# Performance work log

Hardware: AMD Instinct MI355X
Metric: run time of the kernel (lower is better)

Reference implementation:

```python
import jax, jax.numpy as jnp
import numpy as np

INPUT_SIZE = 256
HIDDEN = 64
VOCAB = 8000
B, T = 64, 256


def _lstm_layer(x_seq, W_ih, W_hh, b_ih, b_hh):
    # x_seq: [B, T, D_in]; PyTorch gate order: i, f, g, o
    Bsz = x_seq.shape[0]
    H = W_hh.shape[1]
    # Precompute input projections for all timesteps (one big GEMM)
    x_proj = jnp.einsum('btd,gd->btg', x_seq, W_ih) + b_ih + b_hh  # [B,T,4H]

    def step(carry, xt):
        h, c = carry
        gates = xt + h @ W_hh.T  # [B,4H]
        i, f, g, o = jnp.split(gates, 4, axis=-1)
        i = jax.nn.sigmoid(i)
        f = jax.nn.sigmoid(f)
        g = jnp.tanh(g)
        o = jax.nn.sigmoid(o)
        c = f * c + i * g
        h = o * jnp.tanh(c)
        return (h, c), h

    zeros = jnp.zeros((Bsz, H), x_seq.dtype)
    _, hs = jax.lax.scan(step, (zeros, zeros), jnp.swapaxes(x_proj, 0, 1))
    return jnp.swapaxes(hs, 0, 1)  # [B,T,H]


def setup_inputs() -> dict:
    key = jax.random.key(0)
    ks = jax.random.split(key, 12)
    s0 = 1.0 / np.sqrt(HIDDEN)
    x = jax.random.normal(ks[0], (B, T, INPUT_SIZE), dtype=jnp.float32)
    W_ih0 = jax.random.uniform(ks[1], (4 * HIDDEN, INPUT_SIZE), jnp.float32, -s0, s0)
    W_hh0 = jax.random.uniform(ks[2], (4 * HIDDEN, HIDDEN), jnp.float32, -s0, s0)
    b_ih0 = jax.random.uniform(ks[3], (4 * HIDDEN,), jnp.float32, -s0, s0)
    b_hh0 = jax.random.uniform(ks[4], (4 * HIDDEN,), jnp.float32, -s0, s0)
    W_ih1 = jax.random.uniform(ks[5], (4 * HIDDEN, HIDDEN), jnp.float32, -s0, s0)
    W_hh1 = jax.random.uniform(ks[6], (4 * HIDDEN, HIDDEN), jnp.float32, -s0, s0)
    b_ih1 = jax.random.uniform(ks[7], (4 * HIDDEN,), jnp.float32, -s0, s0)
    b_hh1 = jax.random.uniform(ks[8], (4 * HIDDEN,), jnp.float32, -s0, s0)
    Wl = jax.random.uniform(ks[9], (VOCAB, HIDDEN), jnp.float32, -s0, s0)
    bl = jax.random.uniform(ks[10], (VOCAB,), jnp.float32, -s0, s0)
    return {"x": x, "W_ih0": W_ih0, "W_hh0": W_hh0, "b_ih0": b_ih0, "b_hh0": b_hh0,
            "W_ih1": W_ih1, "W_hh1": W_hh1, "b_ih1": b_ih1, "b_hh1": b_hh1,
            "Wl": Wl, "bl": bl}


def reference(x, W_ih0, W_hh0, b_ih0, b_hh0, W_ih1, W_hh1, b_ih1, b_hh1, Wl, bl):
    h1 = _lstm_layer(x, W_ih0, W_hh0, b_ih0, b_hh0)   # [B,T,H]
    h2 = _lstm_layer(h1, W_ih1, W_hh1, b_ih1, b_hh1)  # [B,T,H]
    return jnp.einsum('bth,vh->btv', h2, Wl) + bl      # [B,T,VOCAB]
```

## Files before the change

kernel.cpp:

```cpp
#include <hip/hip_runtime.h>
#include <math.h>

#define HID 64
#define G4 256
#define TSTEPS 256
#define BATCH 64
#define MTOT 16384
#define NVOCAB 8000

__device__ __forceinline__ float tanh_s(float x){
    float ax = fabsf(x);
    float e = __expf(-2.0f*ax);
    float t = (1.0f - e)/(1.0f + e);
    return x >= 0.f ? t : -t;
}

__global__ void bsum_k(const float* __restrict__ a, const float* __restrict__ b, float* __restrict__ o, int n){
    int i = blockIdx.x*256 + threadIdx.x;
    if (i < n) o[i] = a[i] + b[i];
}

template<int KTOT>
__global__ __launch_bounds__(256, 2) void gemm_bias_nt(
    const float* __restrict__ A, const float* __restrict__ B,
    const float* __restrict__ bias, float* __restrict__ C,
    int M, int N)
{
    __shared__ float As[64][132];
    __shared__ float Bs[64][132];
    const int tid = threadIdx.x;
    const int tx = tid & 15;
    const int ty = tid >> 4;
    const int m0 = blockIdx.y * 128;
    const int n0 = blockIdx.x * 128;

    float4 acc0[8], acc1[8];
    #pragma unroll
    for (int i = 0; i < 8; i++){
        acc0[i] = make_float4(0.f,0.f,0.f,0.f);
        acc1[i] = make_float4(0.f,0.f,0.f,0.f);
    }

    const int rl = tid & 15;
    const int k4 = (tid >> 4) * 4;

    for (int k0 = 0; k0 < KTOT; k0 += 64){
        #pragma unroll
        for (int it = 0; it < 8; it++){
            int r = it*16 + rl;
            float4 va = *(const float4*)(A + (size_t)(m0+r)*KTOT + k0 + k4);
            As[k4+0][r] = va.x; As[k4+1][r] = va.y;
            As[k4+2][r] = va.z; As[k4+3][r] = va.w;
            float4 vb = make_float4(0.f,0.f,0.f,0.f);
            if (n0 + r < N)
                vb = *(const float4*)(B + (size_t)(n0+r)*KTOT + k0 + k4);
            Bs[k4+0][r] = vb.x; Bs[k4+1][r] = vb.y;
            Bs[k4+2][r] = vb.z; Bs[k4+3][r] = vb.w;
        }
        __syncthreads();

        #pragma unroll 8
        for (int k = 0; k < 64; k++){
            float4 a0 = *(const float4*)&As[k][ty*8];
            float4 a1 = *(const float4*)&As[k][ty*8 + 4];
            float4 b0 = *(const float4*)&Bs[k][tx*4];
            float4 b1 = *(const float4*)&Bs[k][64 + tx*4];
            float av[8] = {a0.x,a0.y,a0.z,a0.w,a1.x,a1.y,a1.z,a1.w};
            #pragma unroll
            for (int i = 0; i < 8; i++){
                acc0[i].x = fmaf(av[i], b0.x, acc0[i].x);
                acc0[i].y = fmaf(av[i], b0.y, acc0[i].y);
                acc0[i].z = fmaf(av[i], b0.z, acc0[i].z);
                acc0[i].w = fmaf(av[i], b0.w, acc0[i].w);
                acc1[i].x = fmaf(av[i], b1.x, acc1[i].x);
                acc1[i].y = fmaf(av[i], b1.y, acc1[i].y);
                acc1[i].z = fmaf(av[i], b1.z, acc1[i].z);
                acc1[i].w = fmaf(av[i], b1.w, acc1[i].w);
            }
        }
        __syncthreads();
    }

    const int v0a = n0 + tx*4;
    const int v0b = n0 + 64 + tx*4;
    float4 ba = make_float4(0.f,0.f,0.f,0.f);
    float4 bb = make_float4(0.f,0.f,0.f,0.f);
    if (v0a < N) ba = *(const float4*)(bias + v0a);
    if (v0b < N) bb = *(const float4*)(bias + v0b);
    #pragma unroll
    for (int i = 0; i < 8; i++){
        int m = m0 + ty*8 + i;
        float* crow = C + (size_t)m*N;
        if (v0a < N){
            float4 r;
            r.x = acc0[i].x + ba.x; r.y = acc0[i].y + ba.y;
            r.z = acc0[i].z + ba.z; r.w = acc0[i].w + ba.w;
            *(float4*)(crow + v0a) = r;
        }
        if (v0b < N){
            float4 r;
            r.x = acc1[i].x + bb.x; r.y = acc1[i].y + bb.y;
            r.z = acc1[i].z + bb.z; r.w = acc1[i].w + bb.w;
            *(float4*)(crow + v0b) = r;
        }
    }
}

__global__ __launch_bounds__(256) void lstm_recur(
    const float* __restrict__ XP, const float* __restrict__ Whh,
    float* __restrict__ Hout)
{
    const int b = blockIdx.x;
    const int tid = threadIdx.x;
    const int lane = tid & 63;
    const int wave = tid >> 6;
    const int g  = lane & 3;
    const int j  = wave*16 + (lane >> 2);
    const int row = g*64 + j;
    const bool gb0 = (g & 1) != 0;
    const bool gb1 = (g & 2) != 0;
    const bool is_g = (g == 2);

    __shared__ __align__(16) float hist[TSTEPS+1][HID];

    float4 w[16];
    {
        const float4* wr = (const float4*)(Whh + (size_t)row*HID);
        #pragma unroll
        for (int i = 0; i < 16; i++) w[i] = wr[i];
    }

    if (tid < HID) hist[0][tid] = 0.f;
    __syncthreads();

    const float* xprow = XP + (size_t)b*TSTEPS*G4 + row;
    float xn0 = xprow[0];
    float xn1 = xprow[G4];
    float c = 0.f;

    for (int t = 0; t < TSTEPS; t++){
        float a = xn0;
        xn0 = xn1;
        if (t + 2 < TSTEPS) xn1 = xprow[(size_t)(t+2)*G4];

        const float4* hv = (const float4*)hist[t];
        float s0=0.f, s1=0.f, s2=0.f, s3=0.f;
        #pragma unroll
        for (int i = 0; i < 16; i += 4){
            float4 h0 = hv[i+0];
            float4 h1 = hv[i+1];
            float4 h2 = hv[i+2];
            float4 h3 = hv[i+3];
            s0 = fmaf(w[i+0].x,h0.x,s0); s0 = fmaf(w[i+0].y,h0.y,s0);
            s0 = fmaf(w[i+0].z,h0.z,s0); s0 = fmaf(w[i+0].w,h0.w,s0);
            s1 = fmaf(w[i+1].x,h1.x,s1); s1 = fmaf(w[i+1].y,h1.y,s1);
            s1 = fmaf(w[i+1].z,h1.z,s1); s1 = fmaf(w[i+1].w,h1.w,s1);
            s2 = fmaf(w[i+2].x,h2.x,s2); s2 = fmaf(w[i+2].y,h2.y,s2);
            s2 = fmaf(w[i+2].z,h2.z,s2); s2 = fmaf(w[i+2].w,h2.w,s2);
            s3 = fmaf(w[i+3].x,h3.x,s3); s3 = fmaf(w[i+3].y,h3.y,s3);
            s3 = fmaf(w[i+3].z,h3.z,s3); s3 = fmaf(w[i+3].w,h3.w,s3);
        }
        a += (s0+s1) + (s2+s3);

        float aa = is_g ? 2.f*a : a;
        float sg = 1.f/(1.f + __expf(-aa));
        float act = is_g ? 2.f*sg - 1.f : sg;

        float a1v = __shfl_xor(act, 1, 64);
        float a2v = __shfl_xor(act, 2, 64);
        float a3v = __shfl_xor(act, 3, 64);
        float x0 = gb0 ? a1v : act;
        float x1 = gb0 ? act : a1v;
        float x2 = gb0 ? a3v : a2v;
        float x3 = gb0 ? a2v : a3v;
        float ig = gb1 ? x2 : x0;
        float fg = gb1 ? x3 : x1;
        float gg = gb1 ? x0 : x2;
        float og = gb1 ? x1 : x3;

        c = fmaf(fg, c, ig*gg);
        float hn = og * tanh_s(c);
        if (g == 0) hist[t+1][j] = hn;
        __syncthreads();
    }

    const float4* h4 = (const float4*)&hist[1][0];
    float4* o4 = (float4*)(Hout + (size_t)b*TSTEPS*HID);
    #pragma unroll 4
    for (int i = tid; i < TSTEPS*HID/4; i += 256) o4[i] = h4[i];
}

extern "C" void kernel_launch(void* const* d_in, const int* in_sizes, int n_in,
                              void* d_out, int out_size, void* d_ws, size_t ws_size,
                              hipStream_t stream)
{
    const float* x    = (const float*)d_in[0];
    const float* Wih0 = (const float*)d_in[1];
    const float* Whh0 = (const float*)d_in[2];
    const float* bih0 = (const float*)d_in[3];
    const float* bhh0 = (const float*)d_in[4];
    const float* Wih1 = (const float*)d_in[5];
    const float* Whh1 = (const float*)d_in[6];
    const float* bih1 = (const float*)d_in[7];
    const float* bhh1 = (const float*)d_in[8];
    const float* Wl   = (const float*)d_in[9];
    const float* bl   = (const float*)d_in[10];
    float* out = (float*)d_out;

    float* ws  = (float*)d_ws;
    float* bs0 = ws;
    float* bs1 = bs0 + 256;
    float* xp0 = bs1 + 256;
    float* xp1 = xp0 + 4194304;
    float* h1  = xp1 + 4194304;
    float* h2  = h1  + 1048576;

    bsum_k<<<1, 256, 0, stream>>>(bih0, bhh0, bs0, 256);
    bsum_k<<<1, 256, 0, stream>>>(bih1, bhh1, bs1, 256);

    gemm_bias_nt<256><<<dim3(2,128), 256, 0, stream>>>(x, Wih0, bs0, xp0, MTOT, 256);
    lstm_recur<<<BATCH, 256, 0, stream>>>(xp0, Whh0, h1);

    gemm_bias_nt<64><<<dim3(2,128), 256, 0, stream>>>(h1, Wih1, bs1, xp1, MTOT, 256);
    lstm_recur<<<BATCH, 256, 0, stream>>>(xp1, Whh1, h2);

    gemm_bias_nt<64><<<dim3(63,128), 256, 0, stream>>>(h2, Wl, bl, out, MTOT, NVOCAB);
}
```

Measured before the change: 1.012 ms.

## Fuse both LSTM layers into one wavefront-pipelined kernel and tune output GEMM

Runs the two LSTM layers in a single kernel with 512 threads: the first 256 threads compute layer 1 at step t while the other 256 compute layer 2 at step t-1. Layer 2's input projection is folded into the recurrence through a second register-resident weight set, so the second projection GEMM, its intermediate buffers and one recurrent launch are removed. The two serial recurrences become one pipelined pass of 257 steps, at the cost of more registers per thread and a larger block. The vocab GEMM also switches to BK=32, a higher occupancy hint and nontemporal output stores.

```diff
diff --git a/kernel.cpp b/kernel.cpp
--- a/kernel.cpp
+++ b/kernel.cpp
@@ -8,6 +8,8 @@
 #define MTOT 16384
 #define NVOCAB 8000
 
+typedef float fvec4 __attribute__((ext_vector_type(4)));
+
 __device__ __forceinline__ float tanh_s(float x){
     float ax = fabsf(x);
     float e = __expf(-2.0f*ax);
@@ -15,25 +17,50 @@
     return x >= 0.f ? t : -t;
 }
 
+__device__ __forceinline__ float dot64(const float4* w, const float4* h){
+    float s0=0.f, s1=0.f, s2=0.f, s3=0.f;
+    #pragma unroll
+    for (int i = 0; i < 16; i += 4){
+        float4 h0 = h[i+0];
+        float4 h1 = h[i+1];
+        float4 h2 = h[i+2];
+        float4 h3 = h[i+3];
+        s0 = fmaf(w[i+0].x,h0.x,s0); s0 = fmaf(w[i+0].y,h0.y,s0);
+        s0 = fmaf(w[i+0].z,h0.z,s0); s0 = fmaf(w[i+0].w,h0.w,s0);
+        s1 = fmaf(w[i+1].x,h1.x,s1); s1 = fmaf(w[i+1].y,h1.y,s1);
+        s1 = fmaf(w[i+1].z,h1.z,s1); s1 = fmaf(w[i+1].w,h1.w,s1);
+        s2 = fmaf(w[i+2].x,h2.x,s2); s2 = fmaf(w[i+2].y,h2.y,s2);
+        s2 = fmaf(w[i+2].z,h2.z,s2); s2 = fmaf(w[i+2].w,h2.w,s2);
+        s3 = fmaf(w[i+3].x,h3.x,s3); s3 = fmaf(w[i+3].y,h3.y,s3);
+        s3 = fmaf(w[i+3].z,h3.z,s3); s3 = fmaf(w[i+3].w,h3.w,s3);
+    }
+    return (s0+s1) + (s2+s3);
+}
+
 __global__ void bsum_k(const float* __restrict__ a, const float* __restrict__ b, float* __restrict__ o, int n){
     int i = blockIdx.x*256 + threadIdx.x;
     if (i < n) o[i] = a[i] + b[i];
 }
 
-template<int KTOT>
-__global__ __launch_bounds__(256, 2) void gemm_bias_nt(
+template<int KTOT, int BK, int MINB, bool NTSTORE>
+__global__ __launch_bounds__(256, MINB) void gemm_bias_nt(
     const float* __restrict__ A, const float* __restrict__ B,
     const float* __restrict__ bias, float* __restrict__ C,
     int M, int N)
 {
-    __shared__ float As[64][132];
-    __shared__ float Bs[64][132];
+    __shared__ float As[BK][132];
+    __shared__ float Bs[BK][132];
     const int tid = threadIdx.x;
     const int tx = tid & 15;
     const int ty = tid >> 4;
     const int m0 = blockIdx.y * 128;
     const int n0 = blockIdx.x * 128;
 
+    constexpr int RPP = 1024 / BK;
+    constexpr int NPASS = 128 / RPP;
+    const int rl = tid & (RPP-1);
+    const int k4 = (tid / RPP) * 4;
+
     float4 acc0[8], acc1[8];
     #pragma unroll
     for (int i = 0; i < 8; i++){
@@ -41,13 +68,10 @@
         acc1[i] = make_float4(0.f,0.f,0.f,0.f);
     }
 
-    const int rl = tid & 15;
-    const int k4 = (tid >> 4) * 4;
-
-    for (int k0 = 0; k0 < KTOT; k0 += 64){
+    for (int k0 = 0; k0 < KTOT; k0 += BK){
         #pragma unroll
-        for (int it = 0; it < 8; it++){
-            int r = it*16 + rl;
+        for (int it = 0; it < NPASS; it++){
+            int r = it*RPP + rl;
             float4 va = *(const float4*)(A + (size_t)(m0+r)*KTOT + k0 + k4);
             As[k4+0][r] = va.x; As[k4+1][r] = va.y;
             As[k4+2][r] = va.z; As[k4+3][r] = va.w;
@@ -60,7 +84,7 @@
         __syncthreads();
 
         #pragma unroll 8
-        for (int k = 0; k < 64; k++){
+        for (int k = 0; k < BK; k++){
             float4 a0 = *(const float4*)&As[k][ty*8];
             float4 a1 = *(const float4*)&As[k][ty*8 + 4];
             float4 b0 = *(const float4*)&Bs[k][tx*4];
@@ -92,102 +116,116 @@
         int m = m0 + ty*8 + i;
         float* crow = C + (size_t)m*N;
         if (v0a < N){
-            float4 r;
+            fvec4 r;
             r.x = acc0[i].x + ba.x; r.y = acc0[i].y + ba.y;
             r.z = acc0[i].z + ba.z; r.w = acc0[i].w + ba.w;
-            *(float4*)(crow + v0a) = r;
+            if (NTSTORE) __builtin_nontemporal_store(r, (fvec4*)(crow + v0a));
+            else *(fvec4*)(crow + v0a) = r;
         }
         if (v0b < N){
-            float4 r;
+            fvec4 r;
             r.x = acc1[i].x + bb.x; r.y = acc1[i].y + bb.y;
             r.z = acc1[i].z + bb.z; r.w = acc1[i].w + bb.w;
-            *(float4*)(crow + v0b) = r;
-        }
-    }
-}
-
-__global__ __launch_bounds__(256) void lstm_recur(
-    const float* __restrict__ XP, const float* __restrict__ Whh,
-    float* __restrict__ Hout)
+            if (NTSTORE) __builtin_nontemporal_store(r, (fvec4*)(crow + v0b));
+            else *(fvec4*)(crow + v0b) = r;
+        }
+    }
+}
+
+__global__ __launch_bounds__(512, 2) void lstm_fused(
+    const float* __restrict__ XP,
+    const float* __restrict__ Whh0,
+    const float* __restrict__ Wih1,
+    const float* __restrict__ Whh1,
+    const float* __restrict__ bih1,
+    const float* __restrict__ bhh1,
+    float* __restrict__ H2out)
 {
     const int b = blockIdx.x;
     const int tid = threadIdx.x;
-    const int lane = tid & 63;
-    const int wave = tid >> 6;
+    const bool L1g = tid >= 256;
+    const int t256 = tid & 255;
+    const int lane = t256 & 63;
+    const int w4 = t256 >> 6;
     const int g  = lane & 3;
-    const int j  = wave*16 + (lane >> 2);
+    const int j  = w4*16 + (lane >> 2);
     const int row = g*64 + j;
     const bool gb0 = (g & 1) != 0;
     const bool gb1 = (g & 2) != 0;
     const bool is_g = (g == 2);
 
-    __shared__ __align__(16) float hist[TSTEPS+1][HID];
-
-    float4 w[16];
-    {
-        const float4* wr = (const float4*)(Whh + (size_t)row*HID);
+    __shared__ __align__(16) float h1r[8][HID];
+    __shared__ __align__(16) float hist2[TSTEPS+1][HID];
+
+    float4 wA[16];
+    float4 wB[16];
+    float bias1 = 0.f;
+    if (!L1g){
+        const float4* wr = (const float4*)(Whh0 + (size_t)row*HID);
         #pragma unroll
-        for (int i = 0; i < 16; i++) w[i] = wr[i];
-    }
-
-    if (tid < HID) hist[0][tid] = 0.f;
+        for (int i = 0; i < 16; i++) wA[i] = wr[i];
+    } else {
+        const float4* wr = (const float4*)(Whh1 + (size_t)row*HID);
+        const float4* wi = (const float4*)(Wih1 + (size_t)row*HID);
+        #pragma unroll
+        for (int i = 0; i < 16; i++){ wA[i] = wr[i]; wB[i] = wi[i]; }
+        bias1 = bih1[row] + bhh1[row];
+    }
+
+    if (tid < HID) h1r[0][tid] = 0.f;
+    else if (tid < 2*HID) hist2[0][tid - HID] = 0.f;
     __syncthreads();
 
     const float* xprow = XP + (size_t)b*TSTEPS*G4 + row;
-    float xn0 = xprow[0];
-    float xn1 = xprow[G4];
+    float xn0 = 0.f, xn1 = 0.f;
+    if (!L1g){ xn0 = xprow[0]; xn1 = xprow[G4]; }
     float c = 0.f;
 
-    for (int t = 0; t < TSTEPS; t++){
-        float a = xn0;
-        xn0 = xn1;
-        if (t + 2 < TSTEPS) xn1 = xprow[(size_t)(t+2)*G4];
-
-        const float4* hv = (const float4*)hist[t];
-        float s0=0.f, s1=0.f, s2=0.f, s3=0.f;
-        #pragma unroll
-        for (int i = 0; i < 16; i += 4){
-            float4 h0 = hv[i+0];
-            float4 h1 = hv[i+1];
-            float4 h2 = hv[i+2];
-            float4 h3 = hv[i+3];
-            s0 = fmaf(w[i+0].x,h0.x,s0); s0 = fmaf(w[i+0].y,h0.y,s0);
-            s0 = fmaf(w[i+0].z,h0.z,s0); s0 = fmaf(w[i+0].w,h0.w,s0);
-            s1 = fmaf(w[i+1].x,h1.x,s1); s1 = fmaf(w[i+1].y,h1.y,s1);
-            s1 = fmaf(w[i+1].z,h1.z,s1); s1 = fmaf(w[i+1].w,h1.w,s1);
-            s2 = fmaf(w[i+2].x,h2.x,s2); s2 = fmaf(w[i+2].y,h2.y,s2);
-            s2 = fmaf(w[i+2].z,h2.z,s2); s2 = fmaf(w[i+2].w,h2.w,s2);
-            s3 = fmaf(w[i+3].x,h3.x,s3); s3 = fmaf(w[i+3].y,h3.y,s3);
-            s3 = fmaf(w[i+3].z,h3.z,s3); s3 = fmaf(w[i+3].w,h3.w,s3);
-        }
-        a += (s0+s1) + (s2+s3);
-
-        float aa = is_g ? 2.f*a : a;
-        float sg = 1.f/(1.f + __expf(-aa));
-        float act = is_g ? 2.f*sg - 1.f : sg;
-
-        float a1v = __shfl_xor(act, 1, 64);
-        float a2v = __shfl_xor(act, 2, 64);
-        float a3v = __shfl_xor(act, 3, 64);
-        float x0 = gb0 ? a1v : act;
-        float x1 = gb0 ? act : a1v;
-        float x2 = gb0 ? a3v : a2v;
-        float x3 = gb0 ? a2v : a3v;
-        float ig = gb1 ? x2 : x0;
-        float fg = gb1 ? x3 : x1;
-        float gg = gb1 ? x0 : x2;
-        float og = gb1 ? x1 : x3;
-
-        c = fmaf(fg, c, ig*gg);
-        float hn = og * tanh_s(c);
-        if (g == 0) hist[t+1][j] = hn;
+    for (int t = 0; t <= TSTEPS; t++){
+        const bool active = L1g ? (t >= 1) : (t < TSTEPS);
+        if (active){
+            float a;
+            if (!L1g){
+                a = xn0;
+                xn0 = xn1;
+                if (t + 2 < TSTEPS) xn1 = xprow[(size_t)(t+2)*G4];
+                a += dot64(wA, (const float4*)h1r[t & 7]);
+            } else {
+                a = bias1
+                  + dot64(wB, (const float4*)h1r[t & 7])
+                  + dot64(wA, (const float4*)hist2[t-1]);
+            }
+
+            float aa = is_g ? 2.f*a : a;
+            float sg = 1.f/(1.f + __expf(-aa));
+            float act = is_g ? 2.f*sg - 1.f : sg;
+
+            float a1v = __shfl_xor(act, 1, 64);
+            float a2v = __shfl_xor(act, 2, 64);
+            float a3v = __shfl_xor(act, 3, 64);
+            float x0 = gb0 ? a1v : act;
+            float x1 = gb0 ? act : a1v;
+            float x2 = gb0 ? a3v : a2v;
+            float x3 = gb0 ? a2v : a3v;
+            float ig = gb1 ? x2 : x0;
+            float fg = gb1 ? x3 : x1;
+            float gg = gb1 ? x0 : x2;
+            float og = gb1 ? x1 : x3;
+
+            c = fmaf(fg, c, ig*gg);
+            float hn = og * tanh_s(c);
+            if (g == 0){
+                if (!L1g) h1r[(t+1) & 7][j] = hn;
+                else      hist2[t][j] = hn;
+            }
+        }
         __syncthreads();
     }
 
-    const float4* h4 = (const float4*)&hist[1][0];
-    float4* o4 = (float4*)(Hout + (size_t)b*TSTEPS*HID);
+    const float4* s4 = (const float4*)&hist2[1][0];
+    float4* o4 = (float4*)(H2out + (size_t)b*TSTEPS*HID);
     #pragma unroll 4
-    for (int i = tid; i < TSTEPS*HID/4; i += 256) o4[i] = h4[i];
+    for (int i = tid; i < TSTEPS*HID/4; i += 512) o4[i] = s4[i];
 }
 
 extern "C" void kernel_launch(void* const* d_in, const int* in_sizes, int n_in,
@@ -209,20 +247,14 @@
 
     float* ws  = (float*)d_ws;
     float* bs0 = ws;
-    float* bs1 = bs0 + 256;
-    float* xp0 = bs1 + 256;
-    float* xp1 = xp0 + 4194304;
-    float* h1  = xp1 + 4194304;
-    float* h2  = h1  + 1048576;
+    float* xp0 = bs0 + 256;
+    float* h2  = xp0 + 4194304;
 
     bsum_k<<<1, 256, 0, stream>>>(bih0, bhh0, bs0, 256);
-    bsum_k<<<1, 256, 0, stream>>>(bih1, bhh1, bs1, 256);
-
-    gemm_bias_nt<256><<<dim3(2,128), 256, 0, stream>>>(x, Wih0, bs0, xp0, MTOT, 256);
-    lstm_recur<<<BATCH, 256, 0, stream>>>(xp0, Whh0, h1);
-
-    gemm_bias_nt<64><<<dim3(2,128), 256, 0, stream>>>(h1, Wih1, bs1, xp1, MTOT, 256);
-    lstm_recur<<<BATCH, 256, 0, stream>>>(xp1, Whh1, h2);
-
-    gemm_bias_nt<64><<<dim3(63,128), 256, 0, stream>>>(h2, Wl, bl, out, MTOT, NVOCAB);
-}
+
+    gemm_bias_nt<256,64,2,false><<<dim3(2,128), 256, 0, stream>>>(x, Wih0, bs0, xp0, MTOT, 256);
+
+    lstm_fused<<<BATCH, 512, 0, stream>>>(xp0, Whh0, Wih1, Whh1, bih1, bhh1, h2);
+
+    gemm_bias_nt<64,32,3,true><<<dim3(63,128), 256, 0, stream>>>(h2, Wl, bl, out, MTOT, NVOCAB);
+}
```

Measured after the change: 1.077 ms. 6.4% more time.
